# Optimization experiments

Measured on AMD Instinct MI355X. Metric: run time of the kernel, lower is better.

Reference implementation:

```python
import jax, jax.numpy as jnp
import numpy as np

M, D, G, E = 100000, 64, 1024, 1600000  # nodes, hidden, graphs, edges


def setup_inputs() -> dict:
    key = jax.random.key(0)
    k1, k2, k3, k4 = jax.random.split(key, 4)
    x = jax.random.normal(k1, (M, D), dtype=jnp.float32)
    batch = jnp.sort(jax.random.randint(k2, (M,), 0, G)).astype(jnp.int64)
    edge = jax.random.randint(k3, (2, E), 0, M).astype(jnp.int64)
    # nn.Linear(D, 1) parameters
    att_w = jax.random.normal(k4, (1, D), dtype=jnp.float32) * (1.0 / np.sqrt(D))
    att_b = jnp.zeros((1,), dtype=jnp.float32)
    return {"x": x, "att_w": att_w, "att_b": att_b, "batch": batch, "edge": edge}


def reference(x, att_w, att_b, batch, edge):
    # imp = attention(x): [M, 1] -> [M]
    imp = (x @ att_w.T + att_b)[:, 0]
    # scatter_softmax of imp over graph segments (batch)
    seg_max = jax.ops.segment_max(imp, batch, num_segments=G)
    e = jnp.exp(imp - seg_max[batch])
    denom = jax.ops.segment_sum(e, batch, num_segments=G)
    a = e / denom[batch]  # [M]
    # (degree branch is dead code when degree=False; degree softmax unused)
    # per-node weighted outer product imp_k * x_k x_k^T, scatter-summed per graph
    wj = (a[:, None] * x)[:, :, None] * x[:, None, :]  # [M, D, D]
    out = jax.ops.segment_sum(wj, batch, num_segments=G)  # [G, D, D]
    # Triuvec: upper-triangular (incl. diagonal) vectorization, row-major
    iu = jnp.triu_indices(D)
    return out[:, iu[0], iu[1]]  # [G, D*(D+1)/2]
```

## Files before the change

kernel.cpp:

```cpp
#include <hip/hip_runtime.h>
#include <math.h>


#define DDIM 64
#define NTRI 2080
#define CAP  1024
#define TILE 32

__device__ __forceinline__ float dot_row_w(const float* __restrict__ row,
                                           const float* __restrict__ sW) {
    float d = 0.f;
#pragma unroll
    for (int k = 0; k < 16; ++k) {
        const float4 v = ((const float4*)row)[k];
        const float4 w = ((const float4*)sW)[k];
        d = fmaf(v.x, w.x, d); d = fmaf(v.y, w.y, d);
        d = fmaf(v.z, w.z, d); d = fmaf(v.w, w.w, d);
    }
    return d;
}

__global__ void __launch_bounds__(256)
bounds_kernel(const int* __restrict__ batch, int* __restrict__ seg_start, int M, int G)
{
    const int m = blockIdx.x * 256 + threadIdx.x;
    if (m >= M) return;
    const int b0 = batch[m];
    if (m == 0) {
        for (int g = 0; g <= b0; ++g) seg_start[g] = 0;
    } else {
        const int bp = batch[m - 1];
        for (int g = bp + 1; g <= b0; ++g) seg_start[g] = m;
    }
    if (m == M - 1) {
        for (int g = b0 + 1; g <= G; ++g) seg_start[g] = M;
    }
}

__global__ void __launch_bounds__(256, 4)
sop_kernel(const float* __restrict__ x,
           const float* __restrict__ att_w,
           const float* __restrict__ att_b,
           const int*   __restrict__ seg_start,
           float*       __restrict__ out)
{
    __shared__ __align__(16) float smem[CAP + 4 * TILE * DDIM + DDIM];
    float* sA  = smem;
    float* sXr = smem + CAP;
    float* sYs = smem + CAP + 2 * TILE * DDIM;
    float* sW  = smem + CAP + 4 * TILE * DDIM;
    __shared__ float sRed[8];

    const int g   = blockIdx.x;
    const int tid = threadIdx.x;
    const int s   = seg_start[g];
    const int n   = seg_start[g + 1] - s;
    float* og = out + (size_t)g * NTRI;

    if (n == 0) {
        for (int i = tid; i < NTRI; i += 256) og[i] = 0.f;
        return;
    }

    const int lane16 = tid & 15;
    const int grp    = tid >> 4;
    const float4 wv  = ((const float4*)att_w)[lane16];
    const float  bb  = att_b[0];
    if (tid < DDIM) sW[tid] = att_w[tid];
    const float4* x4 = (const float4*)x;

    for (int idx = grp; idx < n; idx += 16) {
        const float4 v = x4[(size_t)(s + idx) * 16 + lane16];
        float d = fmaf(v.x, wv.x, fmaf(v.y, wv.y, fmaf(v.z, wv.z, v.w * wv.w)));
        d += __shfl_xor(d, 1, 16);
        d += __shfl_xor(d, 2, 16);
        d += __shfl_xor(d, 4, 16);
        d += __shfl_xor(d, 8, 16);
        if (lane16 == 0 && idx < CAP) sA[idx] = d + bb;
    }
    __syncthreads();

    const int wid = tid >> 6, lane = tid & 63;
    float lmax = -INFINITY;
    for (int i = tid; i < n; i += 256) {
        const float d = (i < CAP) ? sA[i] : (dot_row_w(x + (size_t)(s + i) * DDIM, sW) + bb);
        lmax = fmaxf(lmax, d);
    }
#pragma unroll
    for (int off = 32; off > 0; off >>= 1) lmax = fmaxf(lmax, __shfl_down(lmax, off, 64));
    if (lane == 0) sRed[wid] = lmax;
    __syncthreads();
    if (tid == 0) sRed[4] = fmaxf(fmaxf(sRed[0], sRed[1]), fmaxf(sRed[2], sRed[3]));
    __syncthreads();
    const float mx = sRed[4];

    float lsum = 0.f;
    for (int i = tid; i < n; i += 256) {
        const float d  = (i < CAP) ? sA[i] : (dot_row_w(x + (size_t)(s + i) * DDIM, sW) + bb);
        const float ev = __expf(d - mx);
        if (i < CAP) sA[i] = ev;
        lsum += ev;
    }
#pragma unroll
    for (int off = 32; off > 0; off >>= 1) lsum += __shfl_down(lsum, off, 64);
    if (lane == 0) sRed[wid] = lsum;
    __syncthreads();
    if (tid == 0) sRed[5] = 1.0f / (sRed[0] + sRed[1] + sRed[2] + sRed[3]);
    __syncthreads();
    const float inv = sRed[5];
    for (int i = tid; i < n && i < CAP; i += 256) sA[i] *= inv;
    __syncthreads();

    const int i0 = (lane & 7) * 8;
    const int j0 = (lane >> 3) * 8;
    float acc[8][8];
#pragma unroll
    for (int a = 0; a < 8; ++a)
#pragma unroll
        for (int b = 0; b < 8; ++b) acc[a][b] = 0.f;

    const int T = (n + TILE - 1) / TILE;
    float4 r0, r1;
    {
        const int nt0 = min(TILE, n);
        const size_t base = (size_t)s * 16;
        const float4 z = {0.f, 0.f, 0.f, 0.f};
        r0 = (tid       < nt0 * 16) ? x4[base + tid]       : z;
        r1 = (tid + 256 < nt0 * 16) ? x4[base + tid + 256] : z;
    }

    for (int t = 0; t < T; ++t) {
        const int t0  = t * TILE;
        const int nt  = min(TILE, n - t0);
        const int cur = t & 1;
        float* xb = sXr + cur * TILE * DDIM;
        float* yb = sYs + cur * TILE * DDIM;

        {
            const int g0 = t0 + (tid >> 4);
            const int g1 = t0 + ((tid + 256) >> 4);
            float c0 = 0.f, c1 = 0.f;
            if (g0 < n) c0 = (g0 < CAP) ? sA[g0] : __expf(dot_row_w(x + (size_t)(s + g0) * DDIM, sW) + bb - mx) * inv;
            if (g1 < n) c1 = (g1 < CAP) ? sA[g1] : __expf(dot_row_w(x + (size_t)(s + g1) * DDIM, sW) + bb - mx) * inv;
            ((float4*)xb)[tid]       = r0;
            ((float4*)xb)[tid + 256] = r1;
            float4 y0 = {c0 * r0.x, c0 * r0.y, c0 * r0.z, c0 * r0.w};
            float4 y1 = {c1 * r1.x, c1 * r1.y, c1 * r1.z, c1 * r1.w};
            ((float4*)yb)[tid]       = y0;
            ((float4*)yb)[tid + 256] = y1;
        }
        if (t + 1 < T) {
            const int t0n = t0 + TILE;
            const int ntn = min(TILE, n - t0n);
            const size_t base = (size_t)(s + t0n) * 16;
            const float4 z = {0.f, 0.f, 0.f, 0.f};
            r0 = (tid       < ntn * 16) ? x4[base + tid]       : z;
            r1 = (tid + 256 < ntn * 16) ? x4[base + tid + 256] : z;
        }
        __syncthreads();

        for (int nn = wid; nn < nt; nn += 4) {
            float yv[8], xv[8];
            *(float4*)&yv[0] = *(const float4*)&yb[nn * DDIM + i0];
            *(float4*)&yv[4] = *(const float4*)&yb[nn * DDIM + i0 + 4];
            *(float4*)&xv[0] = *(const float4*)&xb[nn * DDIM + j0];
            *(float4*)&xv[4] = *(const float4*)&xb[nn * DDIM + j0 + 4];
#pragma unroll
            for (int a = 0; a < 8; ++a)
#pragma unroll
                for (int b = 0; b < 8; ++b)
                    acc[a][b] = fmaf(yv[a], xv[b], acc[a][b]);
        }
    }
    __syncthreads();

    float* red0 = smem;
    float* red1 = smem + 4096;
    if (wid == 0) {
#pragma unroll
        for (int a = 0; a < 8; ++a) {
            *(float4*)&red0[(i0 + a) * DDIM + j0]     = *(const float4*)&acc[a][0];
            *(float4*)&red0[(i0 + a) * DDIM + j0 + 4] = *(const float4*)&acc[a][4];
        }
    } else if (wid == 1) {
#pragma unroll
        for (int a = 0; a < 8; ++a) {
            *(float4*)&red1[(i0 + a) * DDIM + j0]     = *(const float4*)&acc[a][0];
            *(float4*)&red1[(i0 + a) * DDIM + j0 + 4] = *(const float4*)&acc[a][4];
        }
    }
    __syncthreads();
    if (wid == 2) {
#pragma unroll
        for (int a = 0; a < 8; ++a) {
            float4 u = *(const float4*)&red0[(i0 + a) * DDIM + j0];
            float4 v = *(const float4*)&red0[(i0 + a) * DDIM + j0 + 4];
            u.x += acc[a][0]; u.y += acc[a][1]; u.z += acc[a][2]; u.w += acc[a][3];
            v.x += acc[a][4]; v.y += acc[a][5]; v.z += acc[a][6]; v.w += acc[a][7];
            *(float4*)&red0[(i0 + a) * DDIM + j0]     = u;
            *(float4*)&red0[(i0 + a) * DDIM + j0 + 4] = v;
        }
    } else if (wid == 3) {
#pragma unroll
        for (int a = 0; a < 8; ++a) {
            float4 u = *(const float4*)&red1[(i0 + a) * DDIM + j0];
            float4 v = *(const float4*)&red1[(i0 + a) * DDIM + j0 + 4];
            u.x += acc[a][0]; u.y += acc[a][1]; u.z += acc[a][2]; u.w += acc[a][3];
            v.x += acc[a][4]; v.y += acc[a][5]; v.z += acc[a][6]; v.w += acc[a][7];
            *(float4*)&red1[(i0 + a) * DDIM + j0]     = u;
            *(float4*)&red1[(i0 + a) * DDIM + j0 + 4] = v;
        }
    }
    __syncthreads();

    const int ty = tid >> 4, tx = tid & 15;
    const int fi0 = ty * 4, fj0 = tx * 4;
#pragma unroll
    for (int a = 0; a < 4; ++a) {
        const int i = fi0 + a;
        const int base = i * DDIM - (i * (i - 1)) / 2;
#pragma unroll
        for (int b = 0; b < 4; ++b) {
            const int j = fj0 + b;
            if (j >= i) og[base + (j - i)] = red0[i * DDIM + j] + red1[i * DDIM + j];
        }
    }
}

extern "C" void kernel_launch(void* const* d_in, const int* in_sizes, int n_in,
                              void* d_out, int out_size, void* d_ws, size_t ws_size,
                              hipStream_t stream) {
    const float* x     = (const float*)d_in[0];
    const float* att_w = (const float*)d_in[1];
    const float* att_b = (const float*)d_in[2];
    const int*   batch = (const int*)d_in[3];
    float* out = (float*)d_out;

    const int M = in_sizes[0] / DDIM;
    const int G = out_size / NTRI;

    int* seg_start = (int*)d_ws;

    bounds_kernel<<<(M + 255) / 256, 256, 0, stream>>>(batch, seg_start, M, G);
    sop_kernel<<<G, 256, 0, stream>>>(x, att_w, att_b, seg_start, out);
}
```

Before: 108.5 us.

## Compute per-graph outer-product sums with bf16 MFMA instead of FP32 FMAs

Replaces the FP32 register-tiled outer-product accumulation with MFMA 16x16x32 bf16 instructions. Weighted and unweighted node tiles are packed to bf16 in a swizzled, double-buffered shared-memory layout. Each wave owns a 16-row slice of the 64x64 result, so the cross-wave shared-memory reduction goes away and results are written straight from the accumulators. Rounding inputs to bf16 lowers accuracy, which may exceed tolerance.

```diff
diff --git a/kernel.cpp b/kernel.cpp
--- a/kernel.cpp
+++ b/kernel.cpp
@@ -1,11 +1,15 @@
 #include <hip/hip_runtime.h>
+#include <hip/hip_bf16.h>
 #include <math.h>
 
 
 #define DDIM 64
 #define NTRI 2080
 #define CAP  1024
-#define TILE 32
+#define TK   32
+
+typedef __bf16 bf16x8 __attribute__((ext_vector_type(8)));
+typedef float  f32x4  __attribute__((ext_vector_type(4)));
 
 __device__ __forceinline__ float dot_row_w(const float* __restrict__ row,
                                            const float* __restrict__ sW) {
@@ -18,6 +22,11 @@
         d = fmaf(v.z, w.z, d); d = fmaf(v.w, w.w, d);
     }
     return d;
+}
+
+__device__ __forceinline__ unsigned pack_bf16(float a, float b) {
+    __hip_bfloat162 h2 = __float22bfloat162_rn(make_float2(a, b));
+    return *reinterpret_cast<unsigned*>(&h2);
 }
 
 __global__ void __launch_bounds__(256)
@@ -37,18 +46,16 @@
     }
 }
 
-__global__ void __launch_bounds__(256, 4)
+__global__ void __launch_bounds__(256)
 sop_kernel(const float* __restrict__ x,
            const float* __restrict__ att_w,
            const float* __restrict__ att_b,
            const int*   __restrict__ seg_start,
            float*       __restrict__ out)
 {
-    __shared__ __align__(16) float smem[CAP + 4 * TILE * DDIM + DDIM];
-    float* sA  = smem;
-    float* sXr = smem + CAP;
-    float* sYs = smem + CAP + 2 * TILE * DDIM;
-    float* sW  = smem + CAP + 4 * TILE * DDIM;
+    __shared__ unsigned short sT[2][2][DDIM * TK];
+    __shared__ float sA[CAP];
+    __shared__ float sW[DDIM];
     __shared__ float sRed[8];
 
     const int g   = blockIdx.x;
@@ -63,13 +70,13 @@
     }
 
     const int lane16 = tid & 15;
-    const int grp    = tid >> 4;
+    const int grp16  = tid >> 4;
     const float4 wv  = ((const float4*)att_w)[lane16];
     const float  bb  = att_b[0];
     if (tid < DDIM) sW[tid] = att_w[tid];
     const float4* x4 = (const float4*)x;
 
-    for (int idx = grp; idx < n; idx += 16) {
+    for (int idx = grp16; idx < n; idx += 16) {
         const float4 v = x4[(size_t)(s + idx) * 16 + lane16];
         float d = fmaf(v.x, wv.x, fmaf(v.y, wv.y, fmaf(v.z, wv.z, v.w * wv.w)));
         d += __shfl_xor(d, 1, 16);
@@ -108,121 +115,82 @@
     if (tid == 0) sRed[5] = 1.0f / (sRed[0] + sRed[1] + sRed[2] + sRed[3]);
     __syncthreads();
     const float inv = sRed[5];
-    for (int i = tid; i < n && i < CAP; i += 256) sA[i] *= inv;
-    __syncthreads();
-
-    const int i0 = (lane & 7) * 8;
-    const int j0 = (lane >> 3) * 8;
-    float acc[8][8];
-#pragma unroll
-    for (int a = 0; a < 8; ++a)
-#pragma unroll
-        for (int b = 0; b < 8; ++b) acc[a][b] = 0.f;
-
-    const int T = (n + TILE - 1) / TILE;
-    float4 r0, r1;
+    for (int i = tid; i < CAP && i < n; i += 256) sA[i] *= inv;
+    __syncthreads();
+
+    const int pp = tid & 15;
+    const int cc = tid >> 4;
+    const int il = lane & 15;
+    const int qd = lane >> 4;
+    const int sw = qd ^ ((il >> 1) & 3);
+    const int offA = (16 * wid + il) * TK + (sw << 3);
+    const int offB = il * TK + (sw << 3);
+
+    f32x4 acc[4];
+#pragma unroll
+    for (int jt = 0; jt < 4; ++jt) acc[jt] = (f32x4){0.f, 0.f, 0.f, 0.f};
+
+    const int T = (n + TK - 1) / TK;
+    float4 p0, p1;
     {
-        const int nt0 = min(TILE, n);
-        const size_t base = (size_t)s * 16;
+        const int m0 = 2 * pp;
         const float4 z = {0.f, 0.f, 0.f, 0.f};
-        r0 = (tid       < nt0 * 16) ? x4[base + tid]       : z;
-        r1 = (tid + 256 < nt0 * 16) ? x4[base + tid + 256] : z;
+        p0 = (m0     < n) ? x4[(size_t)(s + m0) * 16 + cc]     : z;
+        p1 = (m0 + 1 < n) ? x4[(size_t)(s + m0 + 1) * 16 + cc] : z;
     }
 
     for (int t = 0; t < T; ++t) {
-        const int t0  = t * TILE;
-        const int nt  = min(TILE, n - t0);
+        const int t0  = t * TK;
         const int cur = t & 1;
-        float* xb = sXr + cur * TILE * DDIM;
-        float* yb = sYs + cur * TILE * DDIM;
-
-        {
-            const int g0 = t0 + (tid >> 4);
-            const int g1 = t0 + ((tid + 256) >> 4);
-            float c0 = 0.f, c1 = 0.f;
-            if (g0 < n) c0 = (g0 < CAP) ? sA[g0] : __expf(dot_row_w(x + (size_t)(s + g0) * DDIM, sW) + bb - mx) * inv;
-            if (g1 < n) c1 = (g1 < CAP) ? sA[g1] : __expf(dot_row_w(x + (size_t)(s + g1) * DDIM, sW) + bb - mx) * inv;
-            ((float4*)xb)[tid]       = r0;
-            ((float4*)xb)[tid + 256] = r1;
-            float4 y0 = {c0 * r0.x, c0 * r0.y, c0 * r0.z, c0 * r0.w};
-            float4 y1 = {c1 * r1.x, c1 * r1.y, c1 * r1.z, c1 * r1.w};
-            ((float4*)yb)[tid]       = y0;
-            ((float4*)yb)[tid + 256] = y1;
-        }
+        unsigned* A32 = (unsigned*)sT[cur][0];
+        unsigned* B32 = (unsigned*)sT[cur][1];
+
+        const int m0 = t0 + 2 * pp;
+        float c0 = 0.f, c1 = 0.f;
+        if (m0 < n)
+            c0 = (m0 < CAP) ? sA[m0]
+               : __expf(dot_row_w(x + (size_t)(s + m0) * DDIM, sW) + bb - mx) * inv;
+        if (m0 + 1 < n)
+            c1 = (m0 + 1 < CAP) ? sA[m0 + 1]
+               : __expf(dot_row_w(x + (size_t)(s + m0 + 1) * DDIM, sW) + bb - mx) * inv;
+
+        const float* f0 = (const float*)&p0;
+        const float* f1 = (const float*)&p1;
+#pragma unroll
+        for (int jf = 0; jf < 4; ++jf) {
+            const int f   = 4 * cc + jf;
+            const int pos = (pp >> 2) ^ ((f >> 1) & 3);
+            const int ui  = f * (TK / 2) + (pos << 2) + (pp & 3);
+            A32[ui] = pack_bf16(c0 * f0[jf], c1 * f1[jf]);
+            B32[ui] = pack_bf16(f0[jf], f1[jf]);
+        }
+
         if (t + 1 < T) {
-            const int t0n = t0 + TILE;
-            const int ntn = min(TILE, n - t0n);
-            const size_t base = (size_t)(s + t0n) * 16;
+            const int m0n = (t + 1) * TK + 2 * pp;
             const float4 z = {0.f, 0.f, 0.f, 0.f};
-            r0 = (tid       < ntn * 16) ? x4[base + tid]       : z;
-            r1 = (tid + 256 < ntn * 16) ? x4[base + tid + 256] : z;
+            p0 = (m0n     < n) ? x4[(size_t)(s + m0n) * 16 + cc]     : z;
+            p1 = (m0n + 1 < n) ? x4[(size_t)(s + m0n + 1) * 16 + cc] : z;
         }
         __syncthreads();
 
-        for (int nn = wid; nn < nt; nn += 4) {
-            float yv[8], xv[8];
-            *(float4*)&yv[0] = *(const float4*)&yb[nn * DDIM + i0];
-            *(float4*)&yv[4] = *(const float4*)&yb[nn * DDIM + i0 + 4];
-            *(float4*)&xv[0] = *(const float4*)&xb[nn * DDIM + j0];
-            *(float4*)&xv[4] = *(const float4*)&xb[nn * DDIM + j0 + 4];
-#pragma unroll
-            for (int a = 0; a < 8; ++a)
-#pragma unroll
-                for (int b = 0; b < 8; ++b)
-                    acc[a][b] = fmaf(yv[a], xv[b], acc[a][b]);
-        }
-    }
-    __syncthreads();
-
-    float* red0 = smem;
-    float* red1 = smem + 4096;
-    if (wid == 0) {
-#pragma unroll
-        for (int a = 0; a < 8; ++a) {
-            *(float4*)&red0[(i0 + a) * DDIM + j0]     = *(const float4*)&acc[a][0];
-            *(float4*)&red0[(i0 + a) * DDIM + j0 + 4] = *(const float4*)&acc[a][4];
-        }
-    } else if (wid == 1) {
-#pragma unroll
-        for (int a = 0; a < 8; ++a) {
-            *(float4*)&red1[(i0 + a) * DDIM + j0]     = *(const float4*)&acc[a][0];
-            *(float4*)&red1[(i0 + a) * DDIM + j0 + 4] = *(const float4*)&acc[a][4];
-        }
-    }
-    __syncthreads();
-    if (wid == 2) {
-#pragma unroll
-        for (int a = 0; a < 8; ++a) {
-            float4 u = *(const float4*)&red0[(i0 + a) * DDIM + j0];
-            float4 v = *(const float4*)&red0[(i0 + a) * DDIM + j0 + 4];
-            u.x += acc[a][0]; u.y += acc[a][1]; u.z += acc[a][2]; u.w += acc[a][3];
-            v.x += acc[a][4]; v.y += acc[a][5]; v.z += acc[a][6]; v.w += acc[a][7];
-            *(float4*)&red0[(i0 + a) * DDIM + j0]     = u;
-            *(float4*)&red0[(i0 + a) * DDIM + j0 + 4] = v;
-        }
-    } else if (wid == 3) {
-#pragma unroll
-        for (int a = 0; a < 8; ++a) {
-            float4 u = *(const float4*)&red1[(i0 + a) * DDIM + j0];
-            float4 v = *(const float4*)&red1[(i0 + a) * DDIM + j0 + 4];
-            u.x += acc[a][0]; u.y += acc[a][1]; u.z += acc[a][2]; u.w += acc[a][3];
-            v.x += acc[a][4]; v.y += acc[a][5]; v.z += acc[a][6]; v.w += acc[a][7];
-            *(float4*)&red1[(i0 + a) * DDIM + j0]     = u;
-            *(float4*)&red1[(i0 + a) * DDIM + j0 + 4] = v;
-        }
-    }
-    __syncthreads();
-
-    const int ty = tid >> 4, tx = tid & 15;
-    const int fi0 = ty * 4, fj0 = tx * 4;
-#pragma unroll
-    for (int a = 0; a < 4; ++a) {
-        const int i = fi0 + a;
-        const int base = i * DDIM - (i * (i - 1)) / 2;
-#pragma unroll
-        for (int b = 0; b < 4; ++b) {
-            const int j = fj0 + b;
-            if (j >= i) og[base + (j - i)] = red0[i * DDIM + j] + red1[i * DDIM + j];
+        const unsigned short* As = sT[cur][0];
+        const unsigned short* Bs = sT[cur][1];
+        const bf16x8 av = *(const bf16x8*)(As + offA);
+#pragma unroll
+        for (int jt = 0; jt < 4; ++jt) {
+            const bf16x8 bv = *(const bf16x8*)(Bs + offB + jt * 16 * TK);
+            acc[jt] = __builtin_amdgcn_mfma_f32_16x16x32_bf16(av, bv, acc[jt], 0, 0, 0);
+        }
+    }
+
+    const int rbase = 16 * wid + qd * 4;
+#pragma unroll
+    for (int jt = 0; jt < 4; ++jt) {
+        const int j = 16 * jt + il;
+#pragma unroll
+        for (int r = 0; r < 4; ++r) {
+            const int i = rbase + r;
+            if (j >= i) og[i * DDIM - (i * (i - 1)) / 2 + (j - i)] = acc[jt][r];
         }
     }
 }
```

Result: faster. 97.71 us (-10.0%).
